# Performance work log

Hardware: AMD Instinct MI355X
Metric: run time of the kernel (lower is better)

The kernel has to match this reference:

```python
import jax, jax.numpy as jnp
import numpy as np

N = 50000
E = 600000
IN_C = 128
HID_C = 128
OUT_C = 128


def _glorot(key, shape):
    fan_in, fan_out = shape[0], shape[1]
    lim = np.sqrt(6.0 / (fan_in + fan_out))
    return jax.random.uniform(key, shape, jnp.float32, -lim, lim)


def setup_inputs() -> dict:
    key = jax.random.key(0)
    ks = jax.random.split(key, 10)
    x = jax.random.normal(ks[0], (N, IN_C), jnp.float32)
    edge_index = jax.random.randint(ks[1], (2, E), 0, N, jnp.int64)
    return {
        "x": x,
        "edge_index": edge_index,
        # SAGEConv1: lin_l (aggregated, with bias) and lin_r (root, no bias)
        "W1_l": _glorot(ks[2], (IN_C, HID_C)),
        "b1_l": jnp.zeros((HID_C,), jnp.float32),
        "W1_r": _glorot(ks[3], (IN_C, HID_C)),
        # SAGEConv2
        "W2_l": _glorot(ks[4], (HID_C, OUT_C)),
        "b2_l": jnp.zeros((OUT_C,), jnp.float32),
        "W2_r": _glorot(ks[5], (HID_C, OUT_C)),
        # final Linear(hidden+out -> out)
        "W_lin": _glorot(ks[6], (HID_C + OUT_C, OUT_C)),
        "b_lin": jnp.zeros((OUT_C,), jnp.float32),
    }


def _sage_conv(x, src, dst, W_l, b_l, W_r):
    # mean-aggregate source features onto destination nodes
    msg = x[src]                                   # [E, C] gather
    agg = jax.ops.segment_sum(msg, dst, num_segments=N)        # [N, C]
    cnt = jax.ops.segment_sum(jnp.ones((src.shape[0],), x.dtype), dst,
                              num_segments=N)                   # [N]
    mean = agg / jnp.maximum(cnt, 1.0)[:, None]
    return mean @ W_l + b_l + x @ W_r


def reference(x, edge_index, W1_l, b1_l, W1_r, W2_l, b2_l, W2_r, W_lin, b_lin):
    src, dst = edge_index[0], edge_index[1]
    x1 = jax.nn.relu(_sage_conv(x, src, dst, W1_l, b1_l, W1_r))   # [N, HID]
    x2 = jax.nn.relu(_sage_conv(x1, src, dst, W2_l, b2_l, W2_r))  # [N, OUT]
    return jnp.concatenate([x1, x2], axis=-1) @ W_lin + b_lin     # [N, OUT]
```

## Files before the change

### kernel.cpp

```cpp
#include <hip/hip_runtime.h>


typedef _Float16 f16;
typedef __attribute__((ext_vector_type(4))) _Float16 f16x4;
typedef __attribute__((ext_vector_type(8))) _Float16 f16x8;
typedef __attribute__((ext_vector_type(4))) float f32x4;

#define RNB 128

__global__ void prep_kernel(const float* __restrict__ x, f16* __restrict__ xh, int n4,
                            const float* __restrict__ W1l, const float* __restrict__ W1r,
                            const float* __restrict__ W2l, const float* __restrict__ W2r,
                            const float* __restrict__ Wlin, f16* __restrict__ wt,
                            int cb) {
  int b = blockIdx.x;
  if (b < cb) {
    int i = b * 256 + threadIdx.x;
    if (i < n4) {
      const float4 v = ((const float4*)x)[i];
      f16x4 h = { (f16)v.x, (f16)v.y, (f16)v.z, (f16)v.w };
      ((f16x4*)xh)[i] = h;
    }
  } else {
    int tid = (b - cb) * 256 + threadIdx.x;
    int w = tid >> 15, idx = tid & 32767;
    int j = idx & 7, n = (idx >> 3) & 127, chunk = idx >> 10;
    int k = chunk * 8 + j;
    float v;
    if (w == 0) v = (k < 128) ? W1l[k * 128 + n] : W1r[(k - 128) * 128 + n];
    else if (w == 1) v = (k < 128) ? W2l[k * 128 + n] : W2r[(k - 128) * 128 + n];
    else v = Wlin[k * 128 + n];
    wt[tid] = (f16)v;
  }
}

__global__ void radix_hist(const int* __restrict__ ei, int* __restrict__ ghist, int E) {
  __shared__ int h[256];
  int tid = threadIdx.x, b = blockIdx.x;
  h[tid] = 0;
  __syncthreads();
  int per = (E + RNB - 1) / RNB;
  int s = b * per, e = s + per; if (e > E) e = E;
  for (int i = s + tid; i < e; i += 256) atomicAdd(&h[ei[E + i] >> 8], 1);
  __syncthreads();
  ghist[tid * RNB + b] = h[tid];
}

__global__ void scan_block_kernel(const int* __restrict__ in, int* __restrict__ out,
                                  int* __restrict__ sums, int n) {
  __shared__ int s[2][1024];
  int t = threadIdx.x;
  int gid = blockIdx.x * 1024 + t;
  int v = (gid < n) ? in[gid] : 0;
  int cur = 0;
  s[0][t] = v;
  __syncthreads();
  for (int ofs = 1; ofs < 1024; ofs <<= 1) {
    int nv = s[cur][t] + ((t >= ofs) ? s[cur][t - ofs] : 0);
    s[cur ^ 1][t] = nv;
    cur ^= 1;
    __syncthreads();
  }
  if (gid < n) out[gid] = s[cur][t] - v;
  if (t == 1023) sums[blockIdx.x] = s[cur][1023];
}

__global__ void scan_add_kernel(int* __restrict__ data, const int* __restrict__ sums, int n) {
  __shared__ int prefix_s;
  int b = blockIdx.x;
  if (threadIdx.x < 64) {
    int v = ((int)threadIdx.x < b) ? sums[threadIdx.x] : 0;
#pragma unroll
    for (int ofs = 1; ofs < 64; ofs <<= 1) v += __shfl_xor(v, ofs);
    if (threadIdx.x == 0) prefix_s = v;
  }
  __syncthreads();
  int gid = b * 1024 + threadIdx.x;
  if (gid < n) data[gid] += prefix_s;
}

__global__ void radix_scatter(const int* __restrict__ ei, const int* __restrict__ sg,
                              int2* __restrict__ tmp, int E) {
  __shared__ int cur[256];
  int tid = threadIdx.x, b = blockIdx.x;
  cur[tid] = sg[tid * RNB + b];
  __syncthreads();
  int per = (E + RNB - 1) / RNB;
  int s = b * per, e = s + per; if (e > E) e = E;
  for (int i = s + tid; i < e; i += 256) {
    int d = ei[E + i], sr = ei[i];
    int pos = atomicAdd(&cur[d >> 8], 1);
    tmp[pos] = make_int2(d, sr);
  }
}

__global__ void radix_bucket(const int2* __restrict__ tmp, const int* __restrict__ sg,
                             int* __restrict__ srcs, int* __restrict__ off,
                             int N, int E, int HB) {
  __shared__ int h[256], sc[256], cur[256];
  int tid = threadIdx.x, hb = blockIdx.x;
  int start = sg[hb * RNB];
  int end = (hb + 1 < HB) ? sg[(hb + 1) * RNB] : E;
  h[tid] = 0;
  __syncthreads();
  for (int i = start + tid; i < end; i += 256) atomicAdd(&h[tmp[i].x & 255], 1);
  __syncthreads();
  sc[tid] = h[tid];
  __syncthreads();
  for (int o = 1; o < 256; o <<= 1) {
    int u = (tid >= o) ? sc[tid - o] : 0;
    __syncthreads();
    sc[tid] += u;
    __syncthreads();
  }
  int excl = sc[tid] - h[tid];
  int v = (hb << 8) + tid;
  if (v < N) off[v] = start + excl;
  if (hb == 0 && tid == 0) off[N] = E;
  cur[tid] = start + excl;
  __syncthreads();
  for (int i = start + tid; i < end; i += 256) {
    int2 p = tmp[i];
    int pos = atomicAdd(&cur[p.x & 255], 1);
    srcs[pos] = p.y;
  }
}

#define AGG_R 6
__global__ void aggregate_kernel(const f16* __restrict__ feat, const int* __restrict__ off,
                                 const int* __restrict__ srcs, f16* __restrict__ meanf, int n) {
  int pair = (int)((blockIdx.x * blockDim.x + threadIdx.x) >> 6);
  int w0 = pair * 2;
  if (w0 >= n) return;
  int w1 = w0 + 1;
  int lane = threadIdx.x & 63;
  int sub = lane >> 4, n15 = lane & 15;
  int beg0 = off[w0], end0 = off[w0 + 1];
  int beg1 = end0;
  int end1 = (w1 < n) ? off[w1 + 1] : end0;
  int deg0 = end0 - beg0, deg1 = end1 - beg1;

  int s0[AGG_R], s1[AGG_R];
  bool v0[AGG_R], v1[AGG_R];
#pragma unroll
  for (int k = 0; k < AGG_R; ++k) {
    int p = 4 * k + sub;
    v0[k] = p < deg0;  s0[k] = v0[k] ? srcs[beg0 + p] : 0;
    v1[k] = p < deg1;  s1[k] = v1[k] ? srcs[beg1 + p] : 0;
  }
  f16x8 g0[AGG_R], g1[AGG_R];
#pragma unroll
  for (int k = 0; k < AGG_R; ++k) {
    if (v0[k]) g0[k] = *(const f16x8*)(feat + (size_t)s0[k] * 128 + n15 * 8);
    if (v1[k]) g1[k] = *(const f16x8*)(feat + (size_t)s1[k] * 128 + n15 * 8);
  }
  float acc0[8] = {}, acc1[8] = {};
#pragma unroll
  for (int k = 0; k < AGG_R; ++k) {
    if (v0[k]) {
#pragma unroll
      for (int j = 0; j < 8; ++j) acc0[j] += (float)g0[k][j];
    }
    if (v1[k]) {
#pragma unroll
      for (int j = 0; j < 8; ++j) acc1[j] += (float)g1[k][j];
    }
  }
  for (int e = beg0 + 4 * AGG_R; e < end0; e += 4) {
    if (sub < end0 - e) {
      int s = srcs[e + sub];
      f16x8 g = *(const f16x8*)(feat + (size_t)s * 128 + n15 * 8);
#pragma unroll
      for (int j = 0; j < 8; ++j) acc0[j] += (float)g[j];
    }
  }
  for (int e = beg1 + 4 * AGG_R; e < end1; e += 4) {
    if (sub < end1 - e) {
      int s = srcs[e + sub];
      f16x8 g = *(const f16x8*)(feat + (size_t)s * 128 + n15 * 8);
#pragma unroll
      for (int j = 0; j < 8; ++j) acc1[j] += (float)g[j];
    }
  }
#pragma unroll
  for (int j = 0; j < 8; ++j) {
    acc0[j] += __shfl_xor(acc0[j], 16);
    acc0[j] += __shfl_xor(acc0[j], 32);
    acc1[j] += __shfl_xor(acc1[j], 16);
    acc1[j] += __shfl_xor(acc1[j], 32);
  }
  if (sub == 0) {
    float inv = 1.0f / fmaxf((float)deg0, 1.0f);
    f16x8 o;
#pragma unroll
    for (int j = 0; j < 8; ++j) o[j] = (f16)(acc0[j] * inv);
    *(f16x8*)(meanf + (size_t)w0 * 128 + n15 * 8) = o;
  } else if (sub == 1 && w1 < n) {
    float inv = 1.0f / fmaxf((float)deg1, 1.0f);
    f16x8 o;
#pragma unroll
    for (int j = 0; j < 8; ++j) o[j] = (f16)(acc1[j] * inv);
    *(f16x8*)(meanf + (size_t)w1 * 128 + n15 * 8) = o;
  }
}

template <bool RELU, bool OUT16>
__global__ __launch_bounds__(256, 4) void gemm_kernel(
    const f16* __restrict__ U, const f16* __restrict__ V, const f16* __restrict__ Wt,
    const float* __restrict__ bias, void* __restrict__ outp, int M) {
  __shared__ f16 ldsb[16384];
  int tid = threadIdx.x;
  int wave = tid >> 6, lane = tid & 63;
  int quad = lane >> 4, n15 = lane & 15;
  int bx = blockIdx.x >> 1, ch = blockIdx.x & 1;
  int m0 = bx * 128 + wave * 32;
  int kq = quad * 8;

  f16x8 a[2][8];
#pragma unroll
  for (int r = 0; r < 2; ++r) {
    int row = m0 + r * 16 + n15;
    int rowc = row < M ? row : M - 1;
    const f16* bu = U + (size_t)rowc * 128 + kq;
    const f16* bv = V + (size_t)rowc * 128 + kq;
#pragma unroll
    for (int kk = 0; kk < 4; ++kk) a[r][kk] = *(const f16x8*)(bu + kk * 32);
#pragma unroll
    for (int kk = 4; kk < 8; ++kk) a[r][kk] = *(const f16x8*)(bv + (kk - 4) * 32);
  }

#pragma unroll
  for (int it = 0; it < 8; ++it) {
    int g = it * 256 + tid;
    int chunk = g >> 6, w64 = g & 63;
    ((f16x8*)ldsb)[g] = ((const f16x8*)Wt)[chunk * 128 + ch * 64 + w64];
  }
  __syncthreads();

  f32x4 acc[2][4] = {};
#pragma unroll
  for (int kk = 0; kk < 8; ++kk) {
#pragma unroll
    for (int t = 0; t < 4; ++t) {
      f16x8 b = ((const f16x8*)ldsb)[(kk * 4 + quad) * 64 + t * 16 + n15];
#pragma unroll
      for (int r = 0; r < 2; ++r)
        acc[r][t] = __builtin_amdgcn_mfma_f32_16x16x32_f16(a[r][kk], b, acc[r][t], 0, 0, 0);
    }
  }

  int rbase0 = m0 + quad * 4;
#pragma unroll
  for (int t = 0; t < 4; ++t) {
    int col = ch * 64 + t * 16 + n15;
    float bv = bias[col];
#pragma unroll
    for (int r = 0; r < 2; ++r) {
#pragma unroll
      for (int i = 0; i < 4; ++i) {
        int row = rbase0 + r * 16 + i;
        if (row < M) {
          float v = acc[r][t][i] + bv;
          if (RELU) v = fmaxf(v, 0.f);
          size_t idx = (size_t)row * 128 + col;
          if (OUT16) ((f16*)outp)[idx] = (f16)v;
          else       ((float*)outp)[idx] = v;
        }
      }
    }
  }
}

extern "C" void kernel_launch(void* const* d_in, const int* in_sizes, int n_in,
                              void* d_out, int out_size, void* d_ws, size_t ws_size,
                              hipStream_t stream) {
  (void)n_in; (void)out_size; (void)ws_size;
  const float* x    = (const float*)d_in[0];
  const int*   ei   = (const int*)d_in[1];
  const float* W1l  = (const float*)d_in[2];
  const float* b1l  = (const float*)d_in[3];
  const float* W1r  = (const float*)d_in[4];
  const float* W2l  = (const float*)d_in[5];
  const float* b2l  = (const float*)d_in[6];
  const float* W2r  = (const float*)d_in[7];
  const float* Wlin = (const float*)d_in[8];
  const float* blin = (const float*)d_in[9];
  const int N = in_sizes[0] / 128;
  const int E = in_sizes[1] / 2;

  char* ws = (char*)d_ws;
  size_t o = 0;
  auto alloc = [&](size_t bytes) {
    char* p = ws + o;
    o = (o + bytes + 255) & ~(size_t)255;
    return p;
  };
  f16*  xh   = (f16*)alloc((size_t)N * 128 * 2);
  f16*  x1h  = (f16*)alloc((size_t)N * 128 * 2);
  f16*  x2h  = (f16*)alloc((size_t)N * 128 * 2);
  f16*  mh   = (f16*)alloc((size_t)N * 128 * 2);
  f16*  wt   = (f16*)alloc((size_t)3 * 32768 * 2);
  int*  off  = (int*)alloc(((size_t)N + 1) * 4);
  int*  srcs = (int*)alloc((size_t)E * 4);
  int2* tmp  = (int2*)alloc((size_t)E * 8);
  int*  ghist= (int*)alloc(256 * RNB * 4);
  int*  sg   = (int*)alloc(256 * RNB * 4);
  int*  sums = (int*)alloc(64 * 4);
  f16* wt1 = wt, *wt2 = wt + 32768, *wt3 = wt + 65536;

  const int n4 = N * 128 / 4;
  const int cb = (n4 + 255) / 256;
  const int wb = (3 * 32768) / 256;
  const int HB = (N + 255) / 256;
  const int SN = 256 * RNB;
  const int snb = SN / 1024;

  radix_hist<<<RNB, 256, 0, stream>>>(ei, ghist, E);
  scan_block_kernel<<<snb, 1024, 0, stream>>>(ghist, sg, sums, SN);
  scan_add_kernel<<<snb, 1024, 0, stream>>>(sg, sums, SN);
  radix_scatter<<<RNB, 256, 0, stream>>>(ei, sg, tmp, E);
  radix_bucket<<<HB, 256, 0, stream>>>(tmp, sg, srcs, off, N, E, HB);

  prep_kernel<<<cb + wb, 256, 0, stream>>>(x, xh, n4, W1l, W1r, W2l, W2r, Wlin, wt, cb);

  const int aggBlocks  = ((N + 1) / 2 + 3) / 4;
  const int gemmBlocks = 2 * ((N + 127) / 128);

  aggregate_kernel<<<aggBlocks, 256, 0, stream>>>(xh, off, srcs, mh, N);
  gemm_kernel<true, true><<<gemmBlocks, 256, 0, stream>>>(mh, xh, wt1, b1l, x1h, N);
  aggregate_kernel<<<aggBlocks, 256, 0, stream>>>(x1h, off, srcs, mh, N);
  gemm_kernel<true, true><<<gemmBlocks, 256, 0, stream>>>(mh, x1h, wt2, b2l, x2h, N);
  gemm_kernel<false, false><<<gemmBlocks, 256, 0, stream>>>(x1h, x2h, wt3, blin, d_out, N);
}
```

Measured before the change: 229.0 us.

## Gather FP8 features in aggregation, fuse prep with histogram, widen GEMM tiles

Node features are now also stored as FP8, so the neighbor-gather aggregation reads half the bytes per edge. x1 is converted by an extra conv8 pass before the second aggregation. The radix histogram is folded into the prep kernel, and scan_add is removed by having the scatter and bucket kernels compute the block-sum prefix themselves. The GEMM now computes all 128 output columns per block, which halves its block count. Storing features in FP8 loses precision and could break the accuracy tolerance, and the added conversion pass costs extra memory traffic.

```diff
diff --git a/kernel.cpp b/kernel.cpp
--- a/kernel.cpp
+++ b/kernel.cpp
@@ -1,18 +1,79 @@
 #include <hip/hip_runtime.h>
+#include <string.h>
 
 
 typedef _Float16 f16;
+typedef unsigned int u32;
 typedef __attribute__((ext_vector_type(4))) _Float16 f16x4;
 typedef __attribute__((ext_vector_type(8))) _Float16 f16x8;
 typedef __attribute__((ext_vector_type(4))) float f32x4;
+typedef __attribute__((ext_vector_type(2))) float f32x2;
 
 #define RNB 128
 
-__global__ void prep_kernel(const float* __restrict__ x, f16* __restrict__ xh, int n4,
+#if __has_builtin(__builtin_amdgcn_cvt_pk_f32_fp8)
+#define DEC_SCALE 1.0f
+__device__ inline void dec4(u32 v, float* o) {
+  f32x2 a = __builtin_amdgcn_cvt_pk_f32_fp8((int)v, false);
+  f32x2 b = __builtin_amdgcn_cvt_pk_f32_fp8((int)v, true);
+  o[0] = a.x; o[1] = a.y; o[2] = b.x; o[3] = b.y;
+}
+#else
+#define DEC_SCALE 256.0f
+__device__ inline void dec4(u32 v, float* o) {
+#pragma unroll
+  for (int i = 0; i < 4; ++i) {
+    u32 byte = (v >> (8 * i)) & 0xffu;
+    union { unsigned short u; _Float16 h; } cv;
+    cv.u = (unsigned short)(((byte & 0x80u) << 8) | ((byte & 0x7fu) << 7));
+    o[i] = (float)cv.h;
+  }
+}
+#endif
+
+#if __has_builtin(__builtin_amdgcn_cvt_pk_fp8_f32)
+__device__ inline u32 enc4(float a, float b, float c, float d) {
+  u32 v = 0;
+  v = (u32)__builtin_amdgcn_cvt_pk_fp8_f32(a, b, (int)v, false);
+  v = (u32)__builtin_amdgcn_cvt_pk_fp8_f32(c, d, (int)v, true);
+  return v;
+}
+#else
+__device__ inline u32 enc1(float x) {
+  union { unsigned short u; _Float16 h; } cv;
+  cv.h = (_Float16)x;
+  u32 hb = cv.u;
+  u32 s = (hb >> 8) & 0x80u;
+  int e = (int)((hb >> 10) & 0x1f);
+  u32 m = hb & 0x3ffu;
+  if (e == 0) return s;
+  int e8 = e - 8;
+  if (e8 <= 0) {
+    int sh = 7 + (1 - e8);
+    u32 full = 0x400u | m;
+    u32 m3 = (sh < 31) ? (full >> sh) : 0;
+    u32 r = (sh - 1 < 31) ? ((full >> (sh - 1)) & 1u) : 0;
+    m3 += r; if (m3 > 7) m3 = 7;
+    return s | m3;
+  }
+  u32 m3 = m >> 7;
+  m3 += (m >> 6) & 1u;
+  if (m3 == 8) { m3 = 0; e8++; }
+  if (e8 >= 16 || (e8 == 15 && m3 == 7)) return s | 0x7Eu;
+  return s | ((u32)e8 << 3) | m3;
+}
+__device__ inline u32 enc4(float a, float b, float c, float d) {
+  return enc1(a) | (enc1(b) << 8) | (enc1(c) << 16) | (enc1(d) << 24);
+}
+#endif
+
+__global__ void prep_kernel(const float* __restrict__ x, f16* __restrict__ xh,
+                            u32* __restrict__ xh8, int n4,
+                            const int* __restrict__ ei, int* __restrict__ ghist, int E,
                             const float* __restrict__ W1l, const float* __restrict__ W1r,
                             const float* __restrict__ W2l, const float* __restrict__ W2r,
                             const float* __restrict__ Wlin, f16* __restrict__ wt,
-                            int cb) {
+                            int cb, int wb) {
   int b = blockIdx.x;
   if (b < cb) {
     int i = b * 256 + threadIdx.x;
@@ -20,8 +81,9 @@
       const float4 v = ((const float4*)x)[i];
       f16x4 h = { (f16)v.x, (f16)v.y, (f16)v.z, (f16)v.w };
       ((f16x4*)xh)[i] = h;
-    }
-  } else {
+      xh8[i] = enc4(v.x, v.y, v.z, v.w);
+    }
+  } else if (b < cb + wb) {
     int tid = (b - cb) * 256 + threadIdx.x;
     int w = tid >> 15, idx = tid & 32767;
     int j = idx & 7, n = (idx >> 3) & 127, chunk = idx >> 10;
@@ -31,19 +93,17 @@
     else if (w == 1) v = (k < 128) ? W2l[k * 128 + n] : W2r[(k - 128) * 128 + n];
     else v = Wlin[k * 128 + n];
     wt[tid] = (f16)v;
-  }
-}
-
-__global__ void radix_hist(const int* __restrict__ ei, int* __restrict__ ghist, int E) {
-  __shared__ int h[256];
-  int tid = threadIdx.x, b = blockIdx.x;
-  h[tid] = 0;
-  __syncthreads();
-  int per = (E + RNB - 1) / RNB;
-  int s = b * per, e = s + per; if (e > E) e = E;
-  for (int i = s + tid; i < e; i += 256) atomicAdd(&h[ei[E + i] >> 8], 1);
-  __syncthreads();
-  ghist[tid * RNB + b] = h[tid];
+  } else {
+    __shared__ int h[256];
+    int tid = threadIdx.x, rb = b - cb - wb;
+    h[tid] = 0;
+    __syncthreads();
+    int per = (E + RNB - 1) / RNB;
+    int s = rb * per, e = s + per; if (e > E) e = E;
+    for (int i = s + tid; i < e; i += 256) atomicAdd(&h[ei[E + i] >> 8], 1);
+    __syncthreads();
+    ghist[tid * RNB + rb] = h[tid];
+  }
 }
 
 __global__ void scan_block_kernel(const int* __restrict__ in, int* __restrict__ out,
@@ -65,25 +125,28 @@
   if (t == 1023) sums[blockIdx.x] = s[cur][1023];
 }
 
-__global__ void scan_add_kernel(int* __restrict__ data, const int* __restrict__ sums, int n) {
-  __shared__ int prefix_s;
-  int b = blockIdx.x;
-  if (threadIdx.x < 64) {
-    int v = ((int)threadIdx.x < b) ? sums[threadIdx.x] : 0;
-#pragma unroll
-    for (int ofs = 1; ofs < 64; ofs <<= 1) v += __shfl_xor(v, ofs);
-    if (threadIdx.x == 0) prefix_s = v;
-  }
-  __syncthreads();
-  int gid = b * 1024 + threadIdx.x;
-  if (gid < n) data[gid] += prefix_s;
+__device__ inline void sums_prefix(const int* sums, int* pf) {
+  int t = threadIdx.x;
+  if (t < 32) {
+    int v = sums[t];
+    int incl = v;
+#pragma unroll
+    for (int ofs = 1; ofs < 32; ofs <<= 1) {
+      int u = __shfl_up(incl, ofs);
+      if (t >= ofs) incl += u;
+    }
+    pf[t] = incl - v;
+  }
 }
 
 __global__ void radix_scatter(const int* __restrict__ ei, const int* __restrict__ sg,
-                              int2* __restrict__ tmp, int E) {
+                              const int* __restrict__ sums, int2* __restrict__ tmp, int E) {
   __shared__ int cur[256];
+  __shared__ int pf[32];
   int tid = threadIdx.x, b = blockIdx.x;
-  cur[tid] = sg[tid * RNB + b];
+  sums_prefix(sums, pf);
+  __syncthreads();
+  cur[tid] = sg[tid * RNB + b] + pf[tid >> 3];
   __syncthreads();
   int per = (E + RNB - 1) / RNB;
   int s = b * per, e = s + per; if (e > E) e = E;
@@ -95,12 +158,15 @@
 }
 
 __global__ void radix_bucket(const int2* __restrict__ tmp, const int* __restrict__ sg,
-                             int* __restrict__ srcs, int* __restrict__ off,
-                             int N, int E, int HB) {
+                             const int* __restrict__ sums, int* __restrict__ srcs,
+                             int* __restrict__ off, int N, int E, int HB) {
   __shared__ int h[256], sc[256], cur[256];
+  __shared__ int pf[32];
   int tid = threadIdx.x, hb = blockIdx.x;
-  int start = sg[hb * RNB];
-  int end = (hb + 1 < HB) ? sg[(hb + 1) * RNB] : E;
+  sums_prefix(sums, pf);
+  __syncthreads();
+  int start = sg[hb * RNB] + pf[hb >> 3];
+  int end = (hb + 1 < HB) ? (sg[(hb + 1) * RNB] + pf[(hb + 1) >> 3]) : E;
   h[tid] = 0;
   __syncthreads();
   for (int i = start + tid; i < end; i += 256) atomicAdd(&h[tmp[i].x & 255], 1);
@@ -126,94 +192,113 @@
   }
 }
 
-#define AGG_R 6
-__global__ void aggregate_kernel(const f16* __restrict__ feat, const int* __restrict__ off,
-                                 const int* __restrict__ srcs, f16* __restrict__ meanf, int n) {
+#define AGG_R8 3
+__global__ void aggregate8_kernel(const uint4* __restrict__ feat8, const int* __restrict__ off,
+                                  const int* __restrict__ srcs, f16* __restrict__ meanf, int n) {
   int pair = (int)((blockIdx.x * blockDim.x + threadIdx.x) >> 6);
   int w0 = pair * 2;
   if (w0 >= n) return;
   int w1 = w0 + 1;
   int lane = threadIdx.x & 63;
-  int sub = lane >> 4, n15 = lane & 15;
+  int sub = lane >> 3, c8 = lane & 7;
   int beg0 = off[w0], end0 = off[w0 + 1];
   int beg1 = end0;
   int end1 = (w1 < n) ? off[w1 + 1] : end0;
   int deg0 = end0 - beg0, deg1 = end1 - beg1;
 
-  int s0[AGG_R], s1[AGG_R];
-  bool v0[AGG_R], v1[AGG_R];
-#pragma unroll
-  for (int k = 0; k < AGG_R; ++k) {
-    int p = 4 * k + sub;
+  int s0[AGG_R8], s1[AGG_R8];
+  bool v0[AGG_R8], v1[AGG_R8];
+#pragma unroll
+  for (int k = 0; k < AGG_R8; ++k) {
+    int p = 8 * k + sub;
     v0[k] = p < deg0;  s0[k] = v0[k] ? srcs[beg0 + p] : 0;
     v1[k] = p < deg1;  s1[k] = v1[k] ? srcs[beg1 + p] : 0;
   }
-  f16x8 g0[AGG_R], g1[AGG_R];
-#pragma unroll
-  for (int k = 0; k < AGG_R; ++k) {
-    if (v0[k]) g0[k] = *(const f16x8*)(feat + (size_t)s0[k] * 128 + n15 * 8);
-    if (v1[k]) g1[k] = *(const f16x8*)(feat + (size_t)s1[k] * 128 + n15 * 8);
-  }
-  float acc0[8] = {}, acc1[8] = {};
-#pragma unroll
-  for (int k = 0; k < AGG_R; ++k) {
+  uint4 g0[AGG_R8], g1[AGG_R8];
+#pragma unroll
+  for (int k = 0; k < AGG_R8; ++k) {
+    if (v0[k]) g0[k] = feat8[s0[k] * 8 + c8];
+    if (v1[k]) g1[k] = feat8[s1[k] * 8 + c8];
+  }
+  float acc0[16] = {}, acc1[16] = {};
+#pragma unroll
+  for (int k = 0; k < AGG_R8; ++k) {
+    float d[16];
     if (v0[k]) {
-#pragma unroll
-      for (int j = 0; j < 8; ++j) acc0[j] += (float)g0[k][j];
+      dec4(g0[k].x, d); dec4(g0[k].y, d + 4); dec4(g0[k].z, d + 8); dec4(g0[k].w, d + 12);
+#pragma unroll
+      for (int j = 0; j < 16; ++j) acc0[j] += d[j];
     }
     if (v1[k]) {
-#pragma unroll
-      for (int j = 0; j < 8; ++j) acc1[j] += (float)g1[k][j];
-    }
-  }
-  for (int e = beg0 + 4 * AGG_R; e < end0; e += 4) {
+      dec4(g1[k].x, d); dec4(g1[k].y, d + 4); dec4(g1[k].z, d + 8); dec4(g1[k].w, d + 12);
+#pragma unroll
+      for (int j = 0; j < 16; ++j) acc1[j] += d[j];
+    }
+  }
+  for (int e = beg0 + 8 * AGG_R8; e < end0; e += 8) {
     if (sub < end0 - e) {
-      int s = srcs[e + sub];
-      f16x8 g = *(const f16x8*)(feat + (size_t)s * 128 + n15 * 8);
-#pragma unroll
-      for (int j = 0; j < 8; ++j) acc0[j] += (float)g[j];
-    }
-  }
-  for (int e = beg1 + 4 * AGG_R; e < end1; e += 4) {
+      uint4 g = feat8[srcs[e + sub] * 8 + c8];
+      float d[16];
+      dec4(g.x, d); dec4(g.y, d + 4); dec4(g.z, d + 8); dec4(g.w, d + 12);
+#pragma unroll
+      for (int j = 0; j < 16; ++j) acc0[j] += d[j];
+    }
+  }
+  for (int e = beg1 + 8 * AGG_R8; e < end1; e += 8) {
     if (sub < end1 - e) {
-      int s = srcs[e + sub];
-      f16x8 g = *(const f16x8*)(feat + (size_t)s * 128 + n15 * 8);
-#pragma unroll
-      for (int j = 0; j < 8; ++j) acc1[j] += (float)g[j];
-    }
-  }
-#pragma unroll
-  for (int j = 0; j < 8; ++j) {
+      uint4 g = feat8[srcs[e + sub] * 8 + c8];
+      float d[16];
+      dec4(g.x, d); dec4(g.y, d + 4); dec4(g.z, d + 8); dec4(g.w, d + 12);
+#pragma unroll
+      for (int j = 0; j < 16; ++j) acc1[j] += d[j];
+    }
+  }
+#pragma unroll
+  for (int j = 0; j < 16; ++j) {
+    acc0[j] += __shfl_xor(acc0[j], 8);
     acc0[j] += __shfl_xor(acc0[j], 16);
     acc0[j] += __shfl_xor(acc0[j], 32);
+    acc1[j] += __shfl_xor(acc1[j], 8);
     acc1[j] += __shfl_xor(acc1[j], 16);
     acc1[j] += __shfl_xor(acc1[j], 32);
   }
   if (sub == 0) {
-    float inv = 1.0f / fmaxf((float)deg0, 1.0f);
-    f16x8 o;
-#pragma unroll
-    for (int j = 0; j < 8; ++j) o[j] = (f16)(acc0[j] * inv);
-    *(f16x8*)(meanf + (size_t)w0 * 128 + n15 * 8) = o;
+    float inv = DEC_SCALE / fmaxf((float)deg0, 1.0f);
+    f16x8 oa, ob;
+#pragma unroll
+    for (int j = 0; j < 8; ++j) { oa[j] = (f16)(acc0[j] * inv); ob[j] = (f16)(acc0[j + 8] * inv); }
+    *(f16x8*)(meanf + (size_t)w0 * 128 + c8 * 16) = oa;
+    *(f16x8*)(meanf + (size_t)w0 * 128 + c8 * 16 + 8) = ob;
   } else if (sub == 1 && w1 < n) {
-    float inv = 1.0f / fmaxf((float)deg1, 1.0f);
-    f16x8 o;
-#pragma unroll
-    for (int j = 0; j < 8; ++j) o[j] = (f16)(acc1[j] * inv);
-    *(f16x8*)(meanf + (size_t)w1 * 128 + n15 * 8) = o;
+    float inv = DEC_SCALE / fmaxf((float)deg1, 1.0f);
+    f16x8 oa, ob;
+#pragma unroll
+    for (int j = 0; j < 8; ++j) { oa[j] = (f16)(acc1[j] * inv); ob[j] = (f16)(acc1[j + 8] * inv); }
+    *(f16x8*)(meanf + (size_t)w1 * 128 + c8 * 16) = oa;
+    *(f16x8*)(meanf + (size_t)w1 * 128 + c8 * 16 + 8) = ob;
+  }
+}
+
+__global__ void conv8_kernel(const f16* __restrict__ in, u32* __restrict__ out, int n8) {
+  int i = blockIdx.x * blockDim.x + threadIdx.x;
+  if (i < n8) {
+    f16x8 v = ((const f16x8*)in)[i];
+    uint2 o;
+    o.x = enc4((float)v[0], (float)v[1], (float)v[2], (float)v[3]);
+    o.y = enc4((float)v[4], (float)v[5], (float)v[6], (float)v[7]);
+    ((uint2*)out)[i] = o;
   }
 }
 
 template <bool RELU, bool OUT16>
-__global__ __launch_bounds__(256, 4) void gemm_kernel(
+__global__ __launch_bounds__(256, 2) void gemm_kernel(
     const f16* __restrict__ U, const f16* __restrict__ V, const f16* __restrict__ Wt,
     const float* __restrict__ bias, void* __restrict__ outp, int M) {
-  __shared__ f16 ldsb[16384];
+  __shared__ f16 ldsb[32768];
   int tid = threadIdx.x;
   int wave = tid >> 6, lane = tid & 63;
   int quad = lane >> 4, n15 = lane & 15;
-  int bx = blockIdx.x >> 1, ch = blockIdx.x & 1;
-  int m0 = bx * 128 + wave * 32;
+  int m0 = blockIdx.x * 128 + wave * 32;
   int kq = quad * 8;
 
   f16x8 a[2][8];
@@ -230,19 +315,18 @@
   }
 
 #pragma unroll
-  for (int it = 0; it < 8; ++it) {
-    int g = it * 256 + tid;
-    int chunk = g >> 6, w64 = g & 63;
-    ((f16x8*)ldsb)[g] = ((const f16x8*)Wt)[chunk * 128 + ch * 64 + w64];
-  }
-  __syncthreads();
-
-  f32x4 acc[2][4] = {};
+  for (int it = 0; it < 16; ++it) {
+    int idx = it * 256 + tid;
+    ((f16x8*)ldsb)[idx] = ((const f16x8*)Wt)[idx];
+  }
+  __syncthreads();
+
+  f32x4 acc[2][8] = {};
 #pragma unroll
   for (int kk = 0; kk < 8; ++kk) {
 #pragma unroll
-    for (int t = 0; t < 4; ++t) {
-      f16x8 b = ((const f16x8*)ldsb)[(kk * 4 + quad) * 64 + t * 16 + n15];
+    for (int t = 0; t < 8; ++t) {
+      f16x8 b = ((const f16x8*)ldsb)[(kk * 4 + quad) * 128 + t * 16 + n15];
 #pragma unroll
       for (int r = 0; r < 2; ++r)
         acc[r][t] = __builtin_amdgcn_mfma_f32_16x16x32_f16(a[r][kk], b, acc[r][t], 0, 0, 0);
@@ -251,9 +335,8 @@
 
   int rbase0 = m0 + quad * 4;
 #pragma unroll
-  for (int t = 0; t < 4; ++t) {
-    int col = ch * 64 + t * 16 + n15;
-    float bv = bias[col];
+  for (int t = 0; t < 8; ++t) {
+    float bv = bias[t * 16 + n15];
 #pragma unroll
     for (int r = 0; r < 2; ++r) {
 #pragma unroll
@@ -262,7 +345,7 @@
         if (row < M) {
           float v = acc[r][t][i] + bv;
           if (RELU) v = fmaxf(v, 0.f);
-          size_t idx = (size_t)row * 128 + col;
+          size_t idx = (size_t)row * 128 + t * 16 + n15;
           if (OUT16) ((f16*)outp)[idx] = (f16)v;
           else       ((float*)outp)[idx] = v;
         }
@@ -299,6 +382,8 @@
   f16*  x1h  = (f16*)alloc((size_t)N * 128 * 2);
   f16*  x2h  = (f16*)alloc((size_t)N * 128 * 2);
   f16*  mh   = (f16*)alloc((size_t)N * 128 * 2);
+  u32*  xh8  = (u32*)alloc((size_t)N * 128);
+  u32*  x1h8 = (u32*)alloc((size_t)N * 128);
   f16*  wt   = (f16*)alloc((size_t)3 * 32768 * 2);
   int*  off  = (int*)alloc(((size_t)N + 1) * 4);
   int*  srcs = (int*)alloc((size_t)E * 4);
@@ -315,20 +400,20 @@
   const int SN = 256 * RNB;
   const int snb = SN / 1024;
 
-  radix_hist<<<RNB, 256, 0, stream>>>(ei, ghist, E);
+  prep_kernel<<<cb + wb + RNB, 256, 0, stream>>>(x, xh, xh8, n4, ei, ghist, E,
+                                                 W1l, W1r, W2l, W2r, Wlin, wt, cb, wb);
   scan_block_kernel<<<snb, 1024, 0, stream>>>(ghist, sg, sums, SN);
-  scan_add_kernel<<<snb, 1024, 0, stream>>>(sg, sums, SN);
-  radix_scatter<<<RNB, 256, 0, stream>>>(ei, sg, tmp, E);
-  radix_bucket<<<HB, 256, 0, stream>>>(tmp, sg, srcs, off, N, E, HB);
-
-  prep_kernel<<<cb + wb, 256, 0, stream>>>(x, xh, n4, W1l, W1r, W2l, W2r, Wlin, wt, cb);
+  radix_scatter<<<RNB, 256, 0, stream>>>(ei, sg, sums, tmp, E);
+  radix_bucket<<<HB, 256, 0, stream>>>(tmp, sg, sums, srcs, off, N, E, HB);
 
   const int aggBlocks  = ((N + 1) / 2 + 3) / 4;
-  const int gemmBlocks = 2 * ((N + 127) / 128);
-
-  aggregate_kernel<<<aggBlocks, 256, 0, stream>>>(xh, off, srcs, mh, N);
+  const int gemmBlocks = (N + 127) / 128;
+  const int c8Blocks   = (N * 128 / 8 + 255) / 256;
+
+  aggregate8_kernel<<<aggBlocks, 256, 0, stream>>>((const uint4*)xh8, off, srcs, mh, N);
   gemm_kernel<true, true><<<gemmBlocks, 256, 0, stream>>>(mh, xh, wt1, b1l, x1h, N);
-  aggregate_kernel<<<aggBlocks, 256, 0, stream>>>(x1h, off, srcs, mh, N);
+  conv8_kernel<<<c8Blocks, 256, 0, stream>>>(x1h, x1h8, N * 128 / 8);
+  aggregate8_kernel<<<aggBlocks, 256, 0, stream>>>((const uint4*)x1h8, off, srcs, mh, N);
   gemm_kernel<true, true><<<gemmBlocks, 256, 0, stream>>>(mh, x1h, wt2, b2l, x2h, N);
   gemm_kernel<false, false><<<gemmBlocks, 256, 0, stream>>>(x1h, x2h, wt3, blin, d_out, N);
 }
```

After: 236.0 us. +3.1%, slower.

## Fuse radix histogram into prep, fold scan-add, slice aggregation, full-width GEMM

Applied to the files above, without the earlier changes.

Merges the radix histogram into the prep kernel and drops the scan_add launch by having scatter and bucket kernels compute the block-sum prefix themselves, cutting the number of launches. Replaces the pair-per-wave aggregation with a feature-slice scheme: four lanes per node each load 8 halves of a 32-column slice, and the slice index comes from the block id. GEMM blocks now compute all 128 output columns, so each A tile is loaded once; in exchange the kernel uses twice the LDS and runs at lower occupancy. The new aggregation loops up to the wave's maximum degree, so lanes whose node has a smaller degree do wasted iterations.

```diff
diff --git a/kernel.cpp b/kernel.cpp
--- a/kernel.cpp
+++ b/kernel.cpp
@@ -9,10 +9,11 @@
 #define RNB 128
 
 __global__ void prep_kernel(const float* __restrict__ x, f16* __restrict__ xh, int n4,
+                            const int* __restrict__ ei, int* __restrict__ ghist, int E,
                             const float* __restrict__ W1l, const float* __restrict__ W1r,
                             const float* __restrict__ W2l, const float* __restrict__ W2r,
                             const float* __restrict__ Wlin, f16* __restrict__ wt,
-                            int cb) {
+                            int cb, int wb) {
   int b = blockIdx.x;
   if (b < cb) {
     int i = b * 256 + threadIdx.x;
@@ -21,7 +22,7 @@
       f16x4 h = { (f16)v.x, (f16)v.y, (f16)v.z, (f16)v.w };
       ((f16x4*)xh)[i] = h;
     }
-  } else {
+  } else if (b < cb + wb) {
     int tid = (b - cb) * 256 + threadIdx.x;
     int w = tid >> 15, idx = tid & 32767;
     int j = idx & 7, n = (idx >> 3) & 127, chunk = idx >> 10;
@@ -31,19 +32,17 @@
     else if (w == 1) v = (k < 128) ? W2l[k * 128 + n] : W2r[(k - 128) * 128 + n];
     else v = Wlin[k * 128 + n];
     wt[tid] = (f16)v;
-  }
-}
-
-__global__ void radix_hist(const int* __restrict__ ei, int* __restrict__ ghist, int E) {
-  __shared__ int h[256];
-  int tid = threadIdx.x, b = blockIdx.x;
-  h[tid] = 0;
-  __syncthreads();
-  int per = (E + RNB - 1) / RNB;
-  int s = b * per, e = s + per; if (e > E) e = E;
-  for (int i = s + tid; i < e; i += 256) atomicAdd(&h[ei[E + i] >> 8], 1);
-  __syncthreads();
-  ghist[tid * RNB + b] = h[tid];
+  } else {
+    __shared__ int h[256];
+    int tid = threadIdx.x, rb = b - cb - wb;
+    h[tid] = 0;
+    __syncthreads();
+    int per = (E + RNB - 1) / RNB;
+    int s = rb * per, e = s + per; if (e > E) e = E;
+    for (int i = s + tid; i < e; i += 256) atomicAdd(&h[ei[E + i] >> 8], 1);
+    __syncthreads();
+    ghist[tid * RNB + rb] = h[tid];
+  }
 }
 
 __global__ void scan_block_kernel(const int* __restrict__ in, int* __restrict__ out,
@@ -65,25 +64,28 @@
   if (t == 1023) sums[blockIdx.x] = s[cur][1023];
 }
 
-__global__ void scan_add_kernel(int* __restrict__ data, const int* __restrict__ sums, int n) {
-  __shared__ int prefix_s;
-  int b = blockIdx.x;
-  if (threadIdx.x < 64) {
-    int v = ((int)threadIdx.x < b) ? sums[threadIdx.x] : 0;
-#pragma unroll
-    for (int ofs = 1; ofs < 64; ofs <<= 1) v += __shfl_xor(v, ofs);
-    if (threadIdx.x == 0) prefix_s = v;
-  }
-  __syncthreads();
-  int gid = b * 1024 + threadIdx.x;
-  if (gid < n) data[gid] += prefix_s;
+__device__ inline void sums_prefix(const int* sums, int* pf) {
+  int t = threadIdx.x;
+  if (t < 32) {
+    int v = sums[t];
+    int incl = v;
+#pragma unroll
+    for (int ofs = 1; ofs < 32; ofs <<= 1) {
+      int u = __shfl_up(incl, ofs);
+      if (t >= ofs) incl += u;
+    }
+    pf[t] = incl - v;
+  }
 }
 
 __global__ void radix_scatter(const int* __restrict__ ei, const int* __restrict__ sg,
-                              int2* __restrict__ tmp, int E) {
+                              const int* __restrict__ sums, int2* __restrict__ tmp, int E) {
   __shared__ int cur[256];
+  __shared__ int pf[32];
   int tid = threadIdx.x, b = blockIdx.x;
-  cur[tid] = sg[tid * RNB + b];
+  sums_prefix(sums, pf);
+  __syncthreads();
+  cur[tid] = sg[tid * RNB + b] + pf[tid >> 3];
   __syncthreads();
   int per = (E + RNB - 1) / RNB;
   int s = b * per, e = s + per; if (e > E) e = E;
@@ -95,12 +97,15 @@
 }
 
 __global__ void radix_bucket(const int2* __restrict__ tmp, const int* __restrict__ sg,
-                             int* __restrict__ srcs, int* __restrict__ off,
-                             int N, int E, int HB) {
+                             const int* __restrict__ sums, int* __restrict__ srcs,
+                             int* __restrict__ off, int N, int E, int HB) {
   __shared__ int h[256], sc[256], cur[256];
+  __shared__ int pf[32];
   int tid = threadIdx.x, hb = blockIdx.x;
-  int start = sg[hb * RNB];
-  int end = (hb + 1 < HB) ? sg[(hb + 1) * RNB] : E;
+  sums_prefix(sums, pf);
+  __syncthreads();
+  int start = sg[hb * RNB] + pf[hb >> 3];
+  int end = (hb + 1 < HB) ? (sg[(hb + 1) * RNB] + pf[(hb + 1) >> 3]) : E;
   h[tid] = 0;
   __syncthreads();
   for (int i = start + tid; i < end; i += 256) atomicAdd(&h[tmp[i].x & 255], 1);
@@ -126,94 +131,69 @@
   }
 }
 
-#define AGG_R 6
-__global__ void aggregate_kernel(const f16* __restrict__ feat, const int* __restrict__ off,
-                                 const int* __restrict__ srcs, f16* __restrict__ meanf, int n) {
-  int pair = (int)((blockIdx.x * blockDim.x + threadIdx.x) >> 6);
-  int w0 = pair * 2;
-  if (w0 >= n) return;
-  int w1 = w0 + 1;
+__global__ void aggregate_slice_kernel(const f16* __restrict__ feat,
+                                       const int* __restrict__ off,
+                                       const int* __restrict__ srcs,
+                                       f16* __restrict__ meanf, int n) {
+  int s = blockIdx.x & 3;
   int lane = threadIdx.x & 63;
-  int sub = lane >> 4, n15 = lane & 15;
-  int beg0 = off[w0], end0 = off[w0 + 1];
-  int beg1 = end0;
-  int end1 = (w1 < n) ? off[w1 + 1] : end0;
-  int deg0 = end0 - beg0, deg1 = end1 - beg1;
-
-  int s0[AGG_R], s1[AGG_R];
-  bool v0[AGG_R], v1[AGG_R];
-#pragma unroll
-  for (int k = 0; k < AGG_R; ++k) {
-    int p = 4 * k + sub;
-    v0[k] = p < deg0;  s0[k] = v0[k] ? srcs[beg0 + p] : 0;
-    v1[k] = p < deg1;  s1[k] = v1[k] ? srcs[beg1 + p] : 0;
-  }
-  f16x8 g0[AGG_R], g1[AGG_R];
-#pragma unroll
-  for (int k = 0; k < AGG_R; ++k) {
-    if (v0[k]) g0[k] = *(const f16x8*)(feat + (size_t)s0[k] * 128 + n15 * 8);
-    if (v1[k]) g1[k] = *(const f16x8*)(feat + (size_t)s1[k] * 128 + n15 * 8);
-  }
-  float acc0[8] = {}, acc1[8] = {};
-#pragma unroll
-  for (int k = 0; k < AGG_R; ++k) {
-    if (v0[k]) {
-#pragma unroll
-      for (int j = 0; j < 8; ++j) acc0[j] += (float)g0[k][j];
-    }
-    if (v1[k]) {
-#pragma unroll
-      for (int j = 0; j < 8; ++j) acc1[j] += (float)g1[k][j];
-    }
-  }
-  for (int e = beg0 + 4 * AGG_R; e < end0; e += 4) {
-    if (sub < end0 - e) {
-      int s = srcs[e + sub];
-      f16x8 g = *(const f16x8*)(feat + (size_t)s * 128 + n15 * 8);
-#pragma unroll
-      for (int j = 0; j < 8; ++j) acc0[j] += (float)g[j];
-    }
-  }
-  for (int e = beg1 + 4 * AGG_R; e < end1; e += 4) {
-    if (sub < end1 - e) {
-      int s = srcs[e + sub];
-      f16x8 g = *(const f16x8*)(feat + (size_t)s * 128 + n15 * 8);
-#pragma unroll
-      for (int j = 0; j < 8; ++j) acc1[j] += (float)g[j];
-    }
-  }
-#pragma unroll
-  for (int j = 0; j < 8; ++j) {
-    acc0[j] += __shfl_xor(acc0[j], 16);
-    acc0[j] += __shfl_xor(acc0[j], 32);
-    acc1[j] += __shfl_xor(acc1[j], 16);
-    acc1[j] += __shfl_xor(acc1[j], 32);
-  }
-  if (sub == 0) {
-    float inv = 1.0f / fmaxf((float)deg0, 1.0f);
+  int node = (blockIdx.x >> 2) * 64 + (threadIdx.x >> 6) * 16 + (lane >> 2);
+  int q = lane & 3;
+  int nc = node < n ? node : n - 1;
+  int beg = off[nc], end = off[nc + 1];
+  int deg = end - beg;
+  int maxd = deg;
+#pragma unroll
+  for (int ofs = 1; ofs < 64; ofs <<= 1) {
+    int o = __shfl_xor(maxd, ofs);
+    maxd = o > maxd ? o : maxd;
+  }
+  const f16* fs = feat + s * 32 + q * 8;
+  float acc[8] = {};
+  for (int r = 0; r < maxd; r += 4) {
+    int i0 = (r + 0 < deg) ? srcs[beg + r + 0] : 0;
+    int i1 = (r + 1 < deg) ? srcs[beg + r + 1] : 0;
+    int i2 = (r + 2 < deg) ? srcs[beg + r + 2] : 0;
+    int i3 = (r + 3 < deg) ? srcs[beg + r + 3] : 0;
+    f16x8 g0 = *(const f16x8*)(fs + (size_t)i0 * 128);
+    f16x8 g1 = *(const f16x8*)(fs + (size_t)i1 * 128);
+    f16x8 g2 = *(const f16x8*)(fs + (size_t)i2 * 128);
+    f16x8 g3 = *(const f16x8*)(fs + (size_t)i3 * 128);
+    if (r + 0 < deg) {
+#pragma unroll
+      for (int j = 0; j < 8; ++j) acc[j] += (float)g0[j];
+    }
+    if (r + 1 < deg) {
+#pragma unroll
+      for (int j = 0; j < 8; ++j) acc[j] += (float)g1[j];
+    }
+    if (r + 2 < deg) {
+#pragma unroll
+      for (int j = 0; j < 8; ++j) acc[j] += (float)g2[j];
+    }
+    if (r + 3 < deg) {
+#pragma unroll
+      for (int j = 0; j < 8; ++j) acc[j] += (float)g3[j];
+    }
+  }
+  if (node < n) {
+    float inv = 1.0f / fmaxf((float)deg, 1.0f);
     f16x8 o;
 #pragma unroll
-    for (int j = 0; j < 8; ++j) o[j] = (f16)(acc0[j] * inv);
-    *(f16x8*)(meanf + (size_t)w0 * 128 + n15 * 8) = o;
-  } else if (sub == 1 && w1 < n) {
-    float inv = 1.0f / fmaxf((float)deg1, 1.0f);
-    f16x8 o;
-#pragma unroll
-    for (int j = 0; j < 8; ++j) o[j] = (f16)(acc1[j] * inv);
-    *(f16x8*)(meanf + (size_t)w1 * 128 + n15 * 8) = o;
+    for (int j = 0; j < 8; ++j) o[j] = (f16)(acc[j] * inv);
+    *(f16x8*)(meanf + (size_t)node * 128 + s * 32 + q * 8) = o;
   }
 }
 
 template <bool RELU, bool OUT16>
-__global__ __launch_bounds__(256, 4) void gemm_kernel(
+__global__ __launch_bounds__(256, 2) void gemm_kernel(
     const f16* __restrict__ U, const f16* __restrict__ V, const f16* __restrict__ Wt,
     const float* __restrict__ bias, void* __restrict__ outp, int M) {
-  __shared__ f16 ldsb[16384];
+  __shared__ f16 ldsb[32768];
   int tid = threadIdx.x;
   int wave = tid >> 6, lane = tid & 63;
   int quad = lane >> 4, n15 = lane & 15;
-  int bx = blockIdx.x >> 1, ch = blockIdx.x & 1;
-  int m0 = bx * 128 + wave * 32;
+  int m0 = blockIdx.x * 128 + wave * 32;
   int kq = quad * 8;
 
   f16x8 a[2][8];
@@ -230,19 +210,18 @@
   }
 
 #pragma unroll
-  for (int it = 0; it < 8; ++it) {
-    int g = it * 256 + tid;
-    int chunk = g >> 6, w64 = g & 63;
-    ((f16x8*)ldsb)[g] = ((const f16x8*)Wt)[chunk * 128 + ch * 64 + w64];
-  }
-  __syncthreads();
-
-  f32x4 acc[2][4] = {};
+  for (int it = 0; it < 16; ++it) {
+    int idx = it * 256 + tid;
+    ((f16x8*)ldsb)[idx] = ((const f16x8*)Wt)[idx];
+  }
+  __syncthreads();
+
+  f32x4 acc[2][8] = {};
 #pragma unroll
   for (int kk = 0; kk < 8; ++kk) {
 #pragma unroll
-    for (int t = 0; t < 4; ++t) {
-      f16x8 b = ((const f16x8*)ldsb)[(kk * 4 + quad) * 64 + t * 16 + n15];
+    for (int t = 0; t < 8; ++t) {
+      f16x8 b = ((const f16x8*)ldsb)[(kk * 4 + quad) * 128 + t * 16 + n15];
 #pragma unroll
       for (int r = 0; r < 2; ++r)
         acc[r][t] = __builtin_amdgcn_mfma_f32_16x16x32_f16(a[r][kk], b, acc[r][t], 0, 0, 0);
@@ -251,9 +230,8 @@
 
   int rbase0 = m0 + quad * 4;
 #pragma unroll
-  for (int t = 0; t < 4; ++t) {
-    int col = ch * 64 + t * 16 + n15;
-    float bv = bias[col];
+  for (int t = 0; t < 8; ++t) {
+    float bv = bias[t * 16 + n15];
 #pragma unroll
     for (int r = 0; r < 2; ++r) {
 #pragma unroll
@@ -262,7 +240,7 @@
         if (row < M) {
           float v = acc[r][t][i] + bv;
           if (RELU) v = fmaxf(v, 0.f);
-          size_t idx = (size_t)row * 128 + col;
+          size_t idx = (size_t)row * 128 + t * 16 + n15;
           if (OUT16) ((f16*)outp)[idx] = (f16)v;
           else       ((float*)outp)[idx] = v;
         }
@@ -315,20 +293,18 @@
   const int SN = 256 * RNB;
   const int snb = SN / 1024;
 
-  radix_hist<<<RNB, 256, 0, stream>>>(ei, ghist, E);
+  prep_kernel<<<cb + wb + RNB, 256, 0, stream>>>(x, xh, n4, ei, ghist, E,
+                                                 W1l, W1r, W2l, W2r, Wlin, wt, cb, wb);
   scan_block_kernel<<<snb, 1024, 0, stream>>>(ghist, sg, sums, SN);
-  scan_add_kernel<<<snb, 1024, 0, stream>>>(sg, sums, SN);
-  radix_scatter<<<RNB, 256, 0, stream>>>(ei, sg, tmp, E);
-  radix_bucket<<<HB, 256, 0, stream>>>(tmp, sg, srcs, off, N, E, HB);
-
-  prep_kernel<<<cb + wb, 256, 0, stream>>>(x, xh, n4, W1l, W1r, W2l, W2r, Wlin, wt, cb);
-
-  const int aggBlocks  = ((N + 1) / 2 + 3) / 4;
-  const int gemmBlocks = 2 * ((N + 127) / 128);
-
-  aggregate_kernel<<<aggBlocks, 256, 0, stream>>>(xh, off, srcs, mh, N);
+  radix_scatter<<<RNB, 256, 0, stream>>>(ei, sg, sums, tmp, E);
+  radix_bucket<<<HB, 256, 0, stream>>>(tmp, sg, sums, srcs, off, N, E, HB);
+
+  const int aggBlocks  = ((N + 63) / 64) * 4;
+  const int gemmBlocks = (N + 127) / 128;
+
+  aggregate_slice_kernel<<<aggBlocks, 256, 0, stream>>>(xh, off, srcs, mh, N);
   gemm_kernel<true, true><<<gemmBlocks, 256, 0, stream>>>(mh, xh, wt1, b1l, x1h, N);
-  aggregate_kernel<<<aggBlocks, 256, 0, stream>>>(x1h, off, srcs, mh, N);
+  aggregate_slice_kernel<<<aggBlocks, 256, 0, stream>>>(x1h, off, srcs, mh, N);
   gemm_kernel<true, true><<<gemmBlocks, 256, 0, stream>>>(mh, x1h, wt2, b2l, x2h, N);
   gemm_kernel<false, false><<<gemmBlocks, 256, 0, stream>>>(x1h, x2h, wt3, blin, d_out, N);
 }
```

Result: slower. 243.0 us (+6.1%).

## Fuse radix histogram into prep, drop scan-add pass, pack sort keys, widen GEMM tiles

Applied to the files above, without the earlier changes.

The radix histogram now runs as extra blocks of the prep kernel, and the scan_add kernel is removed. Each scatter and bucket block instead recomputes the 32-entry block-sum prefix in a wave, which cuts two launches. The sort temporaries are packed into one 32-bit word (src<<8 | low dst bits) instead of an int2, halving that traffic. The GEMM now computes all 128 output columns per block with twice the LDS and lower occupancy, so the A-operand loads are no longer duplicated across two column-half blocks.

```diff
diff --git a/kernel.cpp b/kernel.cpp
--- a/kernel.cpp
+++ b/kernel.cpp
@@ -2,6 +2,7 @@
 
 
 typedef _Float16 f16;
+typedef unsigned int u32;
 typedef __attribute__((ext_vector_type(4))) _Float16 f16x4;
 typedef __attribute__((ext_vector_type(8))) _Float16 f16x8;
 typedef __attribute__((ext_vector_type(4))) float f32x4;
@@ -9,10 +10,11 @@
 #define RNB 128
 
 __global__ void prep_kernel(const float* __restrict__ x, f16* __restrict__ xh, int n4,
+                            const int* __restrict__ ei, int* __restrict__ ghist, int E,
                             const float* __restrict__ W1l, const float* __restrict__ W1r,
                             const float* __restrict__ W2l, const float* __restrict__ W2r,
                             const float* __restrict__ Wlin, f16* __restrict__ wt,
-                            int cb) {
+                            int cb, int wb) {
   int b = blockIdx.x;
   if (b < cb) {
     int i = b * 256 + threadIdx.x;
@@ -21,7 +23,7 @@
       f16x4 h = { (f16)v.x, (f16)v.y, (f16)v.z, (f16)v.w };
       ((f16x4*)xh)[i] = h;
     }
-  } else {
+  } else if (b < cb + wb) {
     int tid = (b - cb) * 256 + threadIdx.x;
     int w = tid >> 15, idx = tid & 32767;
     int j = idx & 7, n = (idx >> 3) & 127, chunk = idx >> 10;
@@ -31,19 +33,17 @@
     else if (w == 1) v = (k < 128) ? W2l[k * 128 + n] : W2r[(k - 128) * 128 + n];
     else v = Wlin[k * 128 + n];
     wt[tid] = (f16)v;
-  }
-}
-
-__global__ void radix_hist(const int* __restrict__ ei, int* __restrict__ ghist, int E) {
-  __shared__ int h[256];
-  int tid = threadIdx.x, b = blockIdx.x;
-  h[tid] = 0;
-  __syncthreads();
-  int per = (E + RNB - 1) / RNB;
-  int s = b * per, e = s + per; if (e > E) e = E;
-  for (int i = s + tid; i < e; i += 256) atomicAdd(&h[ei[E + i] >> 8], 1);
-  __syncthreads();
-  ghist[tid * RNB + b] = h[tid];
+  } else {
+    __shared__ int h[256];
+    int tid = threadIdx.x, rb = b - cb - wb;
+    h[tid] = 0;
+    __syncthreads();
+    int per = (E + RNB - 1) / RNB;
+    int s = rb * per, e = s + per; if (e > E) e = E;
+    for (int i = s + tid; i < e; i += 256) atomicAdd(&h[ei[E + i] >> 8], 1);
+    __syncthreads();
+    ghist[tid * RNB + rb] = h[tid];
+  }
 }
 
 __global__ void scan_block_kernel(const int* __restrict__ in, int* __restrict__ out,
@@ -65,45 +65,51 @@
   if (t == 1023) sums[blockIdx.x] = s[cur][1023];
 }
 
-__global__ void scan_add_kernel(int* __restrict__ data, const int* __restrict__ sums, int n) {
-  __shared__ int prefix_s;
-  int b = blockIdx.x;
-  if (threadIdx.x < 64) {
-    int v = ((int)threadIdx.x < b) ? sums[threadIdx.x] : 0;
-#pragma unroll
-    for (int ofs = 1; ofs < 64; ofs <<= 1) v += __shfl_xor(v, ofs);
-    if (threadIdx.x == 0) prefix_s = v;
-  }
-  __syncthreads();
-  int gid = b * 1024 + threadIdx.x;
-  if (gid < n) data[gid] += prefix_s;
+__device__ inline void sums_prefix(const int* sums, int* pf) {
+  int t = threadIdx.x;
+  if (t < 32) {
+    int v = sums[t];
+    int incl = v;
+#pragma unroll
+    for (int ofs = 1; ofs < 32; ofs <<= 1) {
+      int u = __shfl_up(incl, ofs);
+      if (t >= ofs) incl += u;
+    }
+    pf[t] = incl - v;
+  }
 }
 
 __global__ void radix_scatter(const int* __restrict__ ei, const int* __restrict__ sg,
-                              int2* __restrict__ tmp, int E) {
+                              const int* __restrict__ sums, u32* __restrict__ tmp, int E) {
   __shared__ int cur[256];
+  __shared__ int pf[32];
   int tid = threadIdx.x, b = blockIdx.x;
-  cur[tid] = sg[tid * RNB + b];
+  sums_prefix(sums, pf);
+  __syncthreads();
+  cur[tid] = sg[tid * RNB + b] + pf[tid >> 3];
   __syncthreads();
   int per = (E + RNB - 1) / RNB;
   int s = b * per, e = s + per; if (e > E) e = E;
   for (int i = s + tid; i < e; i += 256) {
     int d = ei[E + i], sr = ei[i];
     int pos = atomicAdd(&cur[d >> 8], 1);
-    tmp[pos] = make_int2(d, sr);
-  }
-}
-
-__global__ void radix_bucket(const int2* __restrict__ tmp, const int* __restrict__ sg,
-                             int* __restrict__ srcs, int* __restrict__ off,
-                             int N, int E, int HB) {
+    tmp[pos] = ((u32)sr << 8) | (u32)(d & 255);
+  }
+}
+
+__global__ void radix_bucket(const u32* __restrict__ tmp, const int* __restrict__ sg,
+                             const int* __restrict__ sums, int* __restrict__ srcs,
+                             int* __restrict__ off, int N, int E, int HB) {
   __shared__ int h[256], sc[256], cur[256];
+  __shared__ int pf[32];
   int tid = threadIdx.x, hb = blockIdx.x;
-  int start = sg[hb * RNB];
-  int end = (hb + 1 < HB) ? sg[(hb + 1) * RNB] : E;
+  sums_prefix(sums, pf);
+  __syncthreads();
+  int start = sg[hb * RNB] + pf[hb >> 3];
+  int end = (hb + 1 < HB) ? (sg[(hb + 1) * RNB] + pf[(hb + 1) >> 3]) : E;
   h[tid] = 0;
   __syncthreads();
-  for (int i = start + tid; i < end; i += 256) atomicAdd(&h[tmp[i].x & 255], 1);
+  for (int i = start + tid; i < end; i += 256) atomicAdd(&h[tmp[i] & 255u], 1);
   __syncthreads();
   sc[tid] = h[tid];
   __syncthreads();
@@ -120,9 +126,9 @@
   cur[tid] = start + excl;
   __syncthreads();
   for (int i = start + tid; i < end; i += 256) {
-    int2 p = tmp[i];
-    int pos = atomicAdd(&cur[p.x & 255], 1);
-    srcs[pos] = p.y;
+    u32 p = tmp[i];
+    int pos = atomicAdd(&cur[p & 255u], 1);
+    srcs[pos] = (int)(p >> 8);
   }
 }
 
@@ -205,15 +211,14 @@
 }
 
 template <bool RELU, bool OUT16>
-__global__ __launch_bounds__(256, 4) void gemm_kernel(
+__global__ __launch_bounds__(256, 2) void gemm_kernel(
     const f16* __restrict__ U, const f16* __restrict__ V, const f16* __restrict__ Wt,
     const float* __restrict__ bias, void* __restrict__ outp, int M) {
-  __shared__ f16 ldsb[16384];
+  __shared__ f16 ldsb[32768];
   int tid = threadIdx.x;
   int wave = tid >> 6, lane = tid & 63;
   int quad = lane >> 4, n15 = lane & 15;
-  int bx = blockIdx.x >> 1, ch = blockIdx.x & 1;
-  int m0 = bx * 128 + wave * 32;
+  int m0 = blockIdx.x * 128 + wave * 32;
   int kq = quad * 8;
 
   f16x8 a[2][8];
@@ -230,19 +235,18 @@
   }
 
 #pragma unroll
-  for (int it = 0; it < 8; ++it) {
-    int g = it * 256 + tid;
-    int chunk = g >> 6, w64 = g & 63;
-    ((f16x8*)ldsb)[g] = ((const f16x8*)Wt)[chunk * 128 + ch * 64 + w64];
-  }
-  __syncthreads();
-
-  f32x4 acc[2][4] = {};
+  for (int it = 0; it < 16; ++it) {
+    int idx = it * 256 + tid;
+    ((f16x8*)ldsb)[idx] = ((const f16x8*)Wt)[idx];
+  }
+  __syncthreads();
+
+  f32x4 acc[2][8] = {};
 #pragma unroll
   for (int kk = 0; kk < 8; ++kk) {
 #pragma unroll
-    for (int t = 0; t < 4; ++t) {
-      f16x8 b = ((const f16x8*)ldsb)[(kk * 4 + quad) * 64 + t * 16 + n15];
+    for (int t = 0; t < 8; ++t) {
+      f16x8 b = ((const f16x8*)ldsb)[(kk * 4 + quad) * 128 + t * 16 + n15];
 #pragma unroll
       for (int r = 0; r < 2; ++r)
         acc[r][t] = __builtin_amdgcn_mfma_f32_16x16x32_f16(a[r][kk], b, acc[r][t], 0, 0, 0);
@@ -251,9 +255,8 @@
 
   int rbase0 = m0 + quad * 4;
 #pragma unroll
-  for (int t = 0; t < 4; ++t) {
-    int col = ch * 64 + t * 16 + n15;
-    float bv = bias[col];
+  for (int t = 0; t < 8; ++t) {
+    float bv = bias[t * 16 + n15];
 #pragma unroll
     for (int r = 0; r < 2; ++r) {
 #pragma unroll
@@ -262,7 +265,7 @@
         if (row < M) {
           float v = acc[r][t][i] + bv;
           if (RELU) v = fmaxf(v, 0.f);
-          size_t idx = (size_t)row * 128 + col;
+          size_t idx = (size_t)row * 128 + t * 16 + n15;
           if (OUT16) ((f16*)outp)[idx] = (f16)v;
           else       ((float*)outp)[idx] = v;
         }
@@ -302,7 +305,7 @@
   f16*  wt   = (f16*)alloc((size_t)3 * 32768 * 2);
   int*  off  = (int*)alloc(((size_t)N + 1) * 4);
   int*  srcs = (int*)alloc((size_t)E * 4);
-  int2* tmp  = (int2*)alloc((size_t)E * 8);
+  u32*  tmp  = (u32*)alloc((size_t)E * 4);
   int*  ghist= (int*)alloc(256 * RNB * 4);
   int*  sg   = (int*)alloc(256 * RNB * 4);
   int*  sums = (int*)alloc(64 * 4);
@@ -315,16 +318,14 @@
   const int SN = 256 * RNB;
   const int snb = SN / 1024;
 
-  radix_hist<<<RNB, 256, 0, stream>>>(ei, ghist, E);
+  prep_kernel<<<cb + wb + RNB, 256, 0, stream>>>(x, xh, n4, ei, ghist, E,
+                                                 W1l, W1r, W2l, W2r, Wlin, wt, cb, wb);
   scan_block_kernel<<<snb, 1024, 0, stream>>>(ghist, sg, sums, SN);
-  scan_add_kernel<<<snb, 1024, 0, stream>>>(sg, sums, SN);
-  radix_scatter<<<RNB, 256, 0, stream>>>(ei, sg, tmp, E);
-  radix_bucket<<<HB, 256, 0, stream>>>(tmp, sg, srcs, off, N, E, HB);
-
-  prep_kernel<<<cb + wb, 256, 0, stream>>>(x, xh, n4, W1l, W1r, W2l, W2r, Wlin, wt, cb);
+  radix_scatter<<<RNB, 256, 0, stream>>>(ei, sg, sums, tmp, E);
+  radix_bucket<<<HB, 256, 0, stream>>>(tmp, sg, sums, srcs, off, N, E, HB);
 
   const int aggBlocks  = ((N + 1) / 2 + 3) / 4;
-  const int gemmBlocks = 2 * ((N + 127) / 128);
+  const int gemmBlocks = (N + 127) / 128;
 
   aggregate_kernel<<<aggBlocks, 256, 0, stream>>>(xh, off, srcs, mh, N);
   gemm_kernel<true, true><<<gemmBlocks, 256, 0, stream>>>(mh, xh, wt1, b1l, x1h, N);
```

Result: no change. 226.8 us (-0.9%).
